# Kernel tuning notes

Measured on AMD Instinct MI355X. Metric: run time of the kernel, lower is better.

The kernel has to match this reference:

```python
import jax, jax.numpy as jnp
import numpy as np

N_HEADS = 16
D_MODEL = 1024
D_HEAD = D_MODEL // N_HEADS  # 64


def setup_inputs() -> dict:
    key = jax.random.key(0)
    ks = jax.random.split(key, 7)
    B, S = 16, 1024
    x = jax.random.normal(ks[0], (B, S, D_MODEL), dtype=jnp.float32)
    # Per-head torch Linear params: weight [out, in] = [D_HEAD, D_HEAD], bias [D_HEAD].
    # Xavier-uniform scale for square weight: sqrt(6/(fan_in+fan_out)).
    lim = float(np.sqrt(6.0 / (D_HEAD + D_HEAD)))
    blim = float(1.0 / np.sqrt(D_HEAD))  # torch default bias init U(-1/sqrt(fan_in), ...)
    Wq = jax.random.uniform(ks[1], (N_HEADS, D_HEAD, D_HEAD), jnp.float32, -lim, lim)
    Wk = jax.random.uniform(ks[2], (N_HEADS, D_HEAD, D_HEAD), jnp.float32, -lim, lim)
    Wv = jax.random.uniform(ks[3], (N_HEADS, D_HEAD, D_HEAD), jnp.float32, -lim, lim)
    bq = jax.random.uniform(ks[4], (N_HEADS, D_HEAD), jnp.float32, -blim, blim)
    bk = jax.random.uniform(ks[5], (N_HEADS, D_HEAD), jnp.float32, -blim, blim)
    bv = jax.random.uniform(ks[6], (N_HEADS, D_HEAD), jnp.float32, -blim, blim)
    return {"sequences": x, "Wq": Wq, "Wk": Wk, "Wv": Wv, "bq": bq, "bk": bk, "bv": bv}


def reference(sequences, Wq, Wk, Wv, bq, bk, bv):
    B, S, D = sequences.shape
    H, dh = N_HEADS, D_HEAD
    # Split feature dim into heads: [B, S, H, dh] (same chunks the torch loop slices).
    x = sequences.reshape(B, S, H, dh)
    # torch Linear: y = x @ W.T + b  -> einsum over the 'in' axis of W[out, in].
    q = jnp.einsum("bshd,hed->bshe", x, Wq) + bq  # [B,S,H,dh]
    k = jnp.einsum("bshd,hed->bshe", x, Wk) + bk
    v = jnp.einsum("bshd,hed->bshe", x, Wv) + bv
    scale = 1.0 / jnp.sqrt(jnp.asarray(dh, dtype=sequences.dtype))
    scores = jnp.einsum("bshe,bthe->bhst", q, k) * scale  # [B,H,S,S]
    weights = jax.nn.softmax(scores, axis=-1)
    attended = jnp.einsum("bhst,bthe->bshe", weights, v)  # [B,S,H,dh]
    # hstack over heads == concat along feature dim.
    return attended.reshape(B, S, D)
```

## Files before the change

kernel.cpp:

```cpp
#include <hip/hip_runtime.h>

constexpr int B_ = 16, S_ = 1024, H_ = 16, DH_ = 64, DM_ = 1024;

typedef short bf16x8 __attribute__((ext_vector_type(8)));
typedef unsigned short us8 __attribute__((ext_vector_type(8)));
typedef unsigned short us4 __attribute__((ext_vector_type(4)));
typedef float f32x4 __attribute__((ext_vector_type(4)));
typedef float f32x16 __attribute__((ext_vector_type(16)));
typedef unsigned u32x4 __attribute__((ext_vector_type(4)));

__device__ __forceinline__ unsigned short f2b(float f) {
    unsigned u = __builtin_bit_cast(unsigned, f);
    u += 0x7FFFu + ((u >> 16) & 1u);
    return (unsigned short)(u >> 16);
}

__device__ __forceinline__ int swz(int r, int c) { return (r << 6) + (c ^ ((r & 7) << 3)); }

__device__ __forceinline__ unsigned cvtpk(float lo, float hi) {
    unsigned r;
    asm("v_cvt_pk_bf16_f32 %0, %1, %2" : "=v"(r) : "v"(lo), "v"(hi));
    return r;
}
__device__ __forceinline__ void permswap(unsigned& a, unsigned& b) {
    asm volatile("v_permlane32_swap_b32 %0, %1" : "+v"(a), "+v"(b));
}

__device__ __forceinline__ void gload16(const unsigned short* g, unsigned short* l) {
    __builtin_amdgcn_global_load_lds(
        (const __attribute__((address_space(1))) void*)g,
        (__attribute__((address_space(3))) void*)l, 16, 0, 0);
}

#define QSCALE 0.18033688011112042f

__global__ __launch_bounds__(256) void proj_kernel(
    const float* __restrict__ x,
    const float* __restrict__ wq, const float* __restrict__ wk, const float* __restrict__ wv,
    const float* __restrict__ bq, const float* __restrict__ bk, const float* __restrict__ bv,
    unsigned short* __restrict__ qo, unsigned short* __restrict__ ko,
    unsigned short* __restrict__ vto)
{
    __shared__ unsigned short xs[128 * 64];
    __shared__ unsigned short wls[3][64 * 64];

    const int tid = threadIdx.x;
    const int bid = blockIdx.x;
    const int chunk = bid & 7, bh = bid >> 3;
    const int b = bh >> 4, h = bh & 15;
    const int s0 = chunk * 128;
    const int lane = tid & 63, w = tid >> 6;
    const int lr = lane & 15, lg = lane >> 4;

    #pragma unroll
    for (int it = 0; it < 4; ++it) {
        int item = it * 256 + tid;
        int row = item >> 3, c = (item & 7) << 3;
        const float* src = x + (size_t)(b * S_ + s0 + row) * DM_ + h * DH_ + c;
        float4 f0 = *(const float4*)src;
        float4 f1 = *(const float4*)(src + 4);
        us8 v = { f2b(f0.x), f2b(f0.y), f2b(f0.z), f2b(f0.w),
                  f2b(f1.x), f2b(f1.y), f2b(f1.z), f2b(f1.w) };
        *(us8*)&xs[swz(row, c)] = v;
    }
    const float* wsrc[3] = { wq, wk, wv };
    #pragma unroll
    for (int mtx = 0; mtx < 3; ++mtx) {
        const float scl = (mtx == 0) ? QSCALE : 1.0f;
        #pragma unroll
        for (int it = 0; it < 2; ++it) {
            int item = it * 256 + tid;
            int row = item >> 3, c = (item & 7) << 3;
            const float* src = wsrc[mtx] + (size_t)h * 4096 + row * 64 + c;
            float4 f0 = *(const float4*)src;
            float4 f1 = *(const float4*)(src + 4);
            us8 v = { f2b(f0.x * scl), f2b(f0.y * scl), f2b(f0.z * scl), f2b(f0.w * scl),
                      f2b(f1.x * scl), f2b(f1.y * scl), f2b(f1.z * scl), f2b(f1.w * scl) };
            *(us8*)&wls[mtx][swz(row, c)] = v;
        }
    }
    __syncthreads();

    bf16x8 af[2][2];
    #pragma unroll
    for (int mt = 0; mt < 2; ++mt)
        #pragma unroll
        for (int k2 = 0; k2 < 2; ++k2)
            af[mt][k2] = *(const bf16x8*)&xs[swz(w * 32 + mt * 16 + lr, k2 * 32 + lg * 8)];

    const float* bias[3] = { bq, bk, bv };
    #pragma unroll
    for (int mtx = 0; mtx < 3; ++mtx) {
        const float bscl = (mtx == 0) ? QSCALE : 1.0f;
        #pragma unroll
        for (int mt = 0; mt < 2; ++mt) {
            #pragma unroll
            for (int n4 = 0; n4 < 4; ++n4) {
                f32x4 acc = { 0.f, 0.f, 0.f, 0.f };
                #pragma unroll
                for (int k2 = 0; k2 < 2; ++k2) {
                    bf16x8 bf_ = *(const bf16x8*)&wls[mtx][swz(n4 * 16 + lr, k2 * 32 + lg * 8)];
                    acc = __builtin_amdgcn_mfma_f32_16x16x32_bf16(af[mt][k2], bf_, acc, 0, 0, 0);
                }
                const int e = n4 * 16 + lr;
                const float bb = bias[mtx][h * DH_ + e] * bscl;
                const int srow0 = s0 + w * 32 + mt * 16 + lg * 4;
                if (mtx == 0) {
                    #pragma unroll
                    for (int r = 0; r < 4; ++r)
                        qo[(size_t)(bh * S_ + srow0 + r) * 64 + e] = f2b(acc[r] + bb);
                } else if (mtx == 1) {
                    #pragma unroll
                    for (int r = 0; r < 4; ++r)
                        ko[(size_t)(bh * S_ + srow0 + r) * 64 + e] = f2b(acc[r] + bb);
                } else {
                    us4 pk = { f2b(acc[0] + bb), f2b(acc[1] + bb),
                               f2b(acc[2] + bb), f2b(acc[3] + bb) };
                    *(us4*)&vto[(size_t)(bh * 64 + e) * S_ + srow0] = pk;
                }
            }
        }
    }
}

__device__ __forceinline__ void qk_tile(const unsigned short* K, const bf16x8 (&qf)[4],
                                        const f32x16& zro, f32x16& p0, f32x16& p1,
                                        int l31, int hi8)
{
    __builtin_amdgcn_s_setprio(1);
    {
        bf16x8 ka0 = *(const bf16x8*)&K[swz(l31,      hi8)];
        bf16x8 ka1 = *(const bf16x8*)&K[swz(32 + l31, hi8)];
        p0 = __builtin_amdgcn_mfma_f32_32x32x16_bf16(ka0, qf[0], zro, 0, 0, 0);
        p1 = __builtin_amdgcn_mfma_f32_32x32x16_bf16(ka1, qf[0], zro, 0, 0, 0);
    }
    #pragma unroll
    for (int s = 1; s < 4; ++s) {
        bf16x8 ka0 = *(const bf16x8*)&K[swz(l31,      s * 16 + hi8)];
        bf16x8 ka1 = *(const bf16x8*)&K[swz(32 + l31, s * 16 + hi8)];
        p0 = __builtin_amdgcn_mfma_f32_32x32x16_bf16(ka0, qf[s], p0, 0, 0, 0);
        p1 = __builtin_amdgcn_mfma_f32_32x32x16_bf16(ka1, qf[s], p1, 0, 0, 0);
    }
    __builtin_amdgcn_s_setprio(0);
}

__device__ __forceinline__ void pv_tile(f32x16& p0, f32x16& p1, const unsigned short* V,
                                        const bf16x8& ones, f32x16& o0, f32x16& o1,
                                        f32x16& lsum, int l31, int hi8)
{
    #pragma unroll
    for (int i = 0; i < 16; ++i) {
        p0[i] = __builtin_amdgcn_exp2f(p0[i]);
        p1[i] = __builtin_amdgcn_exp2f(p1[i]);
    }
    bf16x8 pa[4];
    {
        unsigned a0 = cvtpk(p0[0], p0[1]),  b0 = cvtpk(p0[4], p0[5]);
        unsigned a1 = cvtpk(p0[2], p0[3]),  b1 = cvtpk(p0[6], p0[7]);
        permswap(a0, b0); permswap(a1, b1);
        u32x4 t0 = { a0, a1, b0, b1 };
        pa[0] = __builtin_bit_cast(bf16x8, t0);
        unsigned a2 = cvtpk(p0[8], p0[9]),   b2 = cvtpk(p0[12], p0[13]);
        unsigned a3 = cvtpk(p0[10], p0[11]), b3 = cvtpk(p0[14], p0[15]);
        permswap(a2, b2); permswap(a3, b3);
        u32x4 t1 = { a2, a3, b2, b3 };
        pa[1] = __builtin_bit_cast(bf16x8, t1);
        unsigned a4 = cvtpk(p1[0], p1[1]),  b4 = cvtpk(p1[4], p1[5]);
        unsigned a5 = cvtpk(p1[2], p1[3]),  b5 = cvtpk(p1[6], p1[7]);
        permswap(a4, b4); permswap(a5, b5);
        u32x4 t2 = { a4, a5, b4, b5 };
        pa[2] = __builtin_bit_cast(bf16x8, t2);
        unsigned a6 = cvtpk(p1[8], p1[9]),   b6 = cvtpk(p1[12], p1[13]);
        unsigned a7 = cvtpk(p1[10], p1[11]), b7 = cvtpk(p1[14], p1[15]);
        permswap(a6, b6); permswap(a7, b7);
        u32x4 t3 = { a6, a7, b6, b7 };
        pa[3] = __builtin_bit_cast(bf16x8, t3);
    }
    __builtin_amdgcn_s_setprio(1);
    #pragma unroll
    for (int s = 0; s < 4; ++s) {
        bf16x8 vb0 = *(const bf16x8*)&V[swz(l31,      s * 16 + hi8)];
        bf16x8 vb1 = *(const bf16x8*)&V[swz(32 + l31, s * 16 + hi8)];
        o0 = __builtin_amdgcn_mfma_f32_32x32x16_bf16(pa[s], vb0, o0, 0, 0, 0);
        o1 = __builtin_amdgcn_mfma_f32_32x32x16_bf16(pa[s], vb1, o1, 0, 0, 0);
        lsum = __builtin_amdgcn_mfma_f32_32x32x16_bf16(pa[s], ones, lsum, 0, 0, 0);
    }
    __builtin_amdgcn_s_setprio(0);
}

__global__ __launch_bounds__(256) void attn_kernel(
    const unsigned short* __restrict__ qw, const unsigned short* __restrict__ kw,
    const unsigned short* __restrict__ vtw, float* __restrict__ out)
{
    __shared__ unsigned short ks[3][64 * 64];
    __shared__ unsigned short vs[3][64 * 64];

    const int tid = threadIdx.x, lane = tid & 63, w = tid >> 6;
    int bid = blockIdx.x;
    bid = (bid & 7) * 256 + (bid >> 3);
    const int qt = bid & 7, bh = bid >> 3;
    const int b = bh >> 4, h = bh & 15;
    const int q0 = qt * 128;
    const int l31 = lane & 31, hi = lane >> 5, hi8 = hi << 3;

    const unsigned short* kbase = kw + (size_t)bh * S_ * 64;
    const unsigned short* vbase = vtw + (size_t)bh * 64 * S_;

    const int srow8 = lane >> 3;
    const int colsw = ((lane & 7) ^ (lane >> 3)) << 3;

    auto stage = [&](int t, int bf) {
        const int n1 = t * 64;
        #pragma unroll
        for (int i = 0; i < 2; ++i) {
            const int br = i * 32 + (w << 3);
            gload16(kbase + (size_t)(n1 + br + srow8) * 64 + colsw, &ks[bf][br * 64]);
            gload16(vbase + (size_t)(br + srow8) * S_ + n1 + colsw, &vs[bf][br * 64]);
        }
    };

    bf16x8 qf[4];
    {
        const unsigned short* qp = qw + (size_t)(bh * S_ + q0 + w * 32 + l31) * 64 + hi8;
        #pragma unroll
        for (int s = 0; s < 4; ++s) qf[s] = *(const bf16x8*)(qp + s * 16);
    }

    const short ONE = (short)0x3F80;
    const bf16x8 ones = { ONE, ONE, ONE, ONE, ONE, ONE, ONE, ONE };

    f32x16 o0, o1, lsum, zro;
    #pragma unroll
    for (int i = 0; i < 16; ++i) { o0[i] = 0.f; o1[i] = 0.f; lsum[i] = 0.f; zro[i] = 0.f; }

    stage(0, 0);
    stage(1, 1);
    __syncthreads();

    f32x16 pA0, pA1, pB0, pB1;
    qk_tile(&ks[0][0], qf, zro, pA0, pA1, l31, hi8);

    constexpr int NT = S_ / 64;
    int bT = 0, bT1 = 1, bT2 = 2;
    int t = 0;

    #pragma unroll 1
    for (int tt = 0; tt < 7; ++tt) {
        __syncthreads();
        if (t + 2 < NT) stage(t + 2, bT2);
        qk_tile(&ks[bT1][0], qf, zro, pB0, pB1, l31, hi8);
        pv_tile(pA0, pA1, &vs[bT][0], ones, o0, o1, lsum, l31, hi8);
        { int x = bT; bT = bT1; bT1 = bT2; bT2 = x; } ++t;
        __syncthreads();
        if (t + 2 < NT) stage(t + 2, bT2);
        qk_tile(&ks[bT1][0], qf, zro, pA0, pA1, l31, hi8);
        pv_tile(pB0, pB1, &vs[bT][0], ones, o0, o1, lsum, l31, hi8);
        { int x = bT; bT = bT1; bT1 = bT2; bT2 = x; } ++t;
    }
    __syncthreads();
    qk_tile(&ks[bT1][0], qf, zro, pB0, pB1, l31, hi8);
    pv_tile(pA0, pA1, &vs[bT][0], ones, o0, o1, lsum, l31, hi8);
    { int x = bT; bT = bT1; bT1 = bT2; bT2 = x; }
    pv_tile(pB0, pB1, &vs[bT][0], ones, o0, o1, lsum, l31, hi8);

    #pragma unroll
    for (int r = 0; r < 16; ++r) {
        const int q = (r & 3) + 8 * (r >> 2) + (hi << 2);
        const float iv = 1.0f / lsum[r];
        float* op = out + (size_t)(b * S_ + q0 + w * 32 + q) * DM_ + h * DH_ + l31;
        op[0]  = o0[r] * iv;
        op[32] = o1[r] * iv;
    }
}

extern "C" void kernel_launch(void* const* d_in, const int* in_sizes, int n_in,
                              void* d_out, int out_size, void* d_ws, size_t ws_size,
                              hipStream_t stream) {
    const float* x  = (const float*)d_in[0];
    const float* wq = (const float*)d_in[1];
    const float* wk = (const float*)d_in[2];
    const float* wv = (const float*)d_in[3];
    const float* bq = (const float*)d_in[4];
    const float* bk = (const float*)d_in[5];
    const float* bv = (const float*)d_in[6];
    float* out = (float*)d_out;

    const size_t per = (size_t)B_ * H_ * S_ * DH_;
    unsigned short* qws  = (unsigned short*)d_ws;
    unsigned short* kws  = qws + per;
    unsigned short* vtws = kws + per;

    proj_kernel<<<dim3(2048), dim3(256), 0, stream>>>(x, wq, wk, wv, bq, bk, bv,
                                                      qws, kws, vtws);
    attn_kernel<<<dim3(2048), dim3(256), 0, stream>>>(qws, kws, vtws, out);
}
```

Before: 130.8 us.

## Deepen attention K/V prefetch to four LDS buffers with partial vmcnt waits

Grows the K/V shared-memory ring from three to four stages and prefetches three tiles ahead instead of two. Replaces __syncthreads with an explicit s_waitcnt vmcnt(N) plus barrier, so only the oldest tile's loads must finish and newer prefetches stay in flight. This hides more global-load latency behind MFMA work, at the cost of more LDS per block, which may lower occupancy, and hand-counted vmcnt values that must match the number of outstanding loads.

```diff
diff --git a/kernel.cpp b/kernel.cpp
--- a/kernel.cpp
+++ b/kernel.cpp
@@ -31,6 +31,13 @@
         (const __attribute__((address_space(1))) void*)g,
         (__attribute__((address_space(3))) void*)l, 16, 0, 0);
 }
+
+#define BAR_VM(N) do { \
+    asm volatile("s_waitcnt vmcnt(" #N ") lgkmcnt(0)" ::: "memory"); \
+    __builtin_amdgcn_sched_barrier(0); \
+    __builtin_amdgcn_s_barrier(); \
+    __builtin_amdgcn_sched_barrier(0); \
+} while (0)
 
 #define QSCALE 0.18033688011112042f
 
@@ -192,8 +199,8 @@
     const unsigned short* __restrict__ qw, const unsigned short* __restrict__ kw,
     const unsigned short* __restrict__ vtw, float* __restrict__ out)
 {
-    __shared__ unsigned short ks[3][64 * 64];
-    __shared__ unsigned short vs[3][64 * 64];
+    __shared__ unsigned short ks[4][64 * 64];
+    __shared__ unsigned short vs[4][64 * 64];
 
     const int tid = threadIdx.x, lane = tid & 63, w = tid >> 6;
     int bid = blockIdx.x;
@@ -209,7 +216,8 @@
     const int srow8 = lane >> 3;
     const int colsw = ((lane & 7) ^ (lane >> 3)) << 3;
 
-    auto stage = [&](int t, int bf) {
+    auto stage = [&](int t) {
+        const int bf = t & 3;
         const int n1 = t * 64;
         #pragma unroll
         for (int i = 0; i < 2; ++i) {
@@ -233,35 +241,31 @@
     #pragma unroll
     for (int i = 0; i < 16; ++i) { o0[i] = 0.f; o1[i] = 0.f; lsum[i] = 0.f; zro[i] = 0.f; }
 
-    stage(0, 0);
-    stage(1, 1);
-    __syncthreads();
+    stage(0);
+    stage(1);
+    stage(2);
+    BAR_VM(8);
 
     f32x16 pA0, pA1, pB0, pB1;
     qk_tile(&ks[0][0], qf, zro, pA0, pA1, l31, hi8);
 
     constexpr int NT = S_ / 64;
-    int bT = 0, bT1 = 1, bT2 = 2;
-    int t = 0;
-
     #pragma unroll 1
     for (int tt = 0; tt < 7; ++tt) {
-        __syncthreads();
-        if (t + 2 < NT) stage(t + 2, bT2);
-        qk_tile(&ks[bT1][0], qf, zro, pB0, pB1, l31, hi8);
-        pv_tile(pA0, pA1, &vs[bT][0], ones, o0, o1, lsum, l31, hi8);
-        { int x = bT; bT = bT1; bT1 = bT2; bT2 = x; } ++t;
-        __syncthreads();
-        if (t + 2 < NT) stage(t + 2, bT2);
-        qk_tile(&ks[bT1][0], qf, zro, pA0, pA1, l31, hi8);
-        pv_tile(pB0, pB1, &vs[bT][0], ones, o0, o1, lsum, l31, hi8);
-        { int x = bT; bT = bT1; bT1 = bT2; bT2 = x; } ++t;
-    }
-    __syncthreads();
-    qk_tile(&ks[bT1][0], qf, zro, pB0, pB1, l31, hi8);
-    pv_tile(pA0, pA1, &vs[bT][0], ones, o0, o1, lsum, l31, hi8);
-    { int x = bT; bT = bT1; bT1 = bT2; bT2 = x; }
-    pv_tile(pB0, pB1, &vs[bT][0], ones, o0, o1, lsum, l31, hi8);
+        const int t0 = 2 * tt;
+        BAR_VM(4);
+        stage(t0 + 3);
+        qk_tile(&ks[(t0 + 1) & 3][0], qf, zro, pB0, pB1, l31, hi8);
+        pv_tile(pA0, pA1, &vs[t0 & 3][0], ones, o0, o1, lsum, l31, hi8);
+        BAR_VM(4);
+        if (t0 + 4 < NT) stage(t0 + 4);
+        qk_tile(&ks[(t0 + 2) & 3][0], qf, zro, pA0, pA1, l31, hi8);
+        pv_tile(pB0, pB1, &vs[(t0 + 1) & 3][0], ones, o0, o1, lsum, l31, hi8);
+    }
+    BAR_VM(0);
+    qk_tile(&ks[15 & 3][0], qf, zro, pB0, pB1, l31, hi8);
+    pv_tile(pA0, pA1, &vs[14 & 3][0], ones, o0, o1, lsum, l31, hi8);
+    pv_tile(pB0, pB1, &vs[15 & 3][0], ones, o0, o1, lsum, l31, hi8);
 
     #pragma unroll
     for (int r = 0; r < 16; ++r) {
```

Result: no change. 129.4 us (-1.1%).
